# Kernel optimization log

Measured on AMD Instinct MI355X. Metric: run time of the kernel, lower is better.

The kernel has to match this reference:

```python
import jax, jax.numpy as jnp
import numpy as np

C = 16          # n_channels
HIDDEN = 128
ALPHA_THRESH = 0.1
STEP_SIZE = 1.0


def _perception_kernel():
    ident = jnp.array([[0., 0., 0.], [0., 1., 0.], [0., 0., 0.]], dtype=jnp.float32)
    dx = jnp.array([[-0.125, 0., 0.125], [-0.25, 0., 0.25], [-0.125, 0., 0.125]], dtype=jnp.float32)
    dy = dx.T  # angle = 0 -> no rotation
    k = jnp.stack([ident, dx, dy])                 # [3,3,3]
    return jnp.tile(k, (C, 1, 1))[:, None]          # [3C,1,3,3], OIHW, groups=C


def _wrap_pad(x):
    # circular padding of 1 on H and W (torus)
    return jnp.pad(x, ((0, 0), (0, 0), (1, 1), (1, 1)), mode='wrap')


def _living_mask(x):
    alpha = x[:, 3:4]                               # [B,1,H,W]
    pooled = jax.lax.reduce_window(_wrap_pad(alpha), -jnp.inf, jax.lax.max,
                                   (1, 1, 3, 3), (1, 1, 1, 1), 'VALID')
    return pooled > ALPHA_THRESH                    # [B,1,H,W] bool


def _perceive(x):
    kern = _perception_kernel()
    return jax.lax.conv_general_dilated(
        _wrap_pad(x), kern, window_strides=(1, 1), padding='VALID',
        feature_group_count=C,
        dimension_numbers=('NCHW', 'OIHW', 'NCHW'))   # [B,3C,H,W]


def setup_inputs() -> dict:
    key = jax.random.key(0)
    k1, k2, k3, k4 = jax.random.split(key, 4)
    B, H, W = 32, 256, 256
    x = jax.random.uniform(k1, (B, C, H, W), dtype=jnp.float32)
    fire_mask = jax.random.randint(k2, (B, 1, H, W), 0, 2).astype(jnp.int32)
    # Conv2d(48->128,1) and Conv2d(128->16,1) weights, stored as matrices
    w1 = jax.random.normal(k3, (HIDDEN, 3 * C), dtype=jnp.float32) * (1.0 / np.sqrt(3 * C))
    b1 = jnp.zeros((HIDDEN,), dtype=jnp.float32)
    w2 = jax.random.normal(k4, (C, HIDDEN), dtype=jnp.float32) * (1.0 / np.sqrt(HIDDEN))
    b2 = jnp.zeros((C,), dtype=jnp.float32)
    return {"x": x, "w1": w1, "b1": b1, "w2": w2, "b2": b2, "fire_mask": fire_mask}


def reference(x, w1, b1, w2, b2, fire_mask):
    pre_life = _living_mask(x)                                   # [B,1,H,W]
    y = _perceive(x)                                             # [B,3C,H,W]
    h = jax.nn.relu(jnp.einsum('bchw,oc->bohw', y, w1) + b1[None, :, None, None])
    dx = (jnp.einsum('bchw,oc->bohw', h, w2) + b2[None, :, None, None]) * STEP_SIZE
    dx = dx * fire_mask.astype(dx.dtype)                          # stochastic update mask
    x_new = x + dx
    post_life = _living_mask(x_new)
    life = (pre_life & post_life).astype(x_new.dtype)
    return x_new * life
```

## Files before the change

### kernel.cpp

```cpp
#include <hip/hip_runtime.h>
#include <hip/hip_bf16.h>


#define CCH 16
#define HID 128
#define HH 256
#define WW 256
#define BB 32

typedef __attribute__((ext_vector_type(8))) short bf16x8;
typedef __attribute__((ext_vector_type(4))) float f32x4;
typedef __attribute__((ext_vector_type(4))) int i32x4;
typedef __attribute__((ext_vector_type(2))) unsigned int u32x2;

union bfpack {
  u32x2 w2[2];
  bf16x8 v;
};

__device__ inline unsigned short f2bf(float f) {
  unsigned int u = __float_as_uint(f);
  u += 0x7FFFu + ((u >> 16) & 1u);
  return (unsigned short)(u >> 16);
}
__device__ inline float bf2f(unsigned short s) {
  return __uint_as_float(((unsigned int)s) << 16);
}
__device__ inline unsigned int cvtpk2(float a, float b) {
  union { __hip_bfloat162 h; unsigned int u; } cv;
  cv.h = __float22bfloat162_rn(make_float2(a, b));
  return cv.u;
}

__global__ __launch_bounds__(256) void pack_weights_kernel(
    const float* __restrict__ w1, const float* __restrict__ w2,
    unsigned short* __restrict__ w1p, unsigned short* __restrict__ w2p) {
  const int tid = blockIdx.x * 256 + threadIdx.x;
  if (tid < 2048) {
    const int l = tid & 63, m = (tid >> 6) & 7, ks = (tid >> 9) & 1,
              pl = (tid >> 10) & 1;
    const int row = m * 16 + (l & 15);
    const int kb = ks * 32 + (l >> 4) * 8;
    const size_t off = ((((size_t)pl * 2 + ks) * 8 + m) * 64 + l) * 8;
#pragma unroll
    for (int j = 0; j < 8; ++j) {
      const int k = kb + j;
      const int cc = k >> 2, f = k & 3;
      const float v = (f < 3) ? w1[row * 48 + cc * 3 + f] : 0.0f;
      const unsigned short hi = f2bf(v);
      w1p[off + j] = (pl == 0) ? hi : f2bf(v - bf2f(hi));
    }
  } else if (tid < 2560) {
    const int t2 = tid - 2048;
    const int l = t2 & 63, ks = (t2 >> 6) & 3, pl = (t2 >> 8) & 1;
    const int row = l & 15;
    const int kb = ks * 32 + (l >> 4) * 8;
    const size_t off = (((size_t)pl * 4 + ks) * 64 + l) * 8;
#pragma unroll
    for (int j = 0; j < 8; ++j) {
      const float v = w2[row * 128 + kb + j];
      const unsigned short hi = f2bf(v);
      w2p[off + j] = (pl == 0) ? hi : f2bf(v - bf2f(hi));
    }
  }
}

__device__ inline int swkey(int row) {
  return (((row >> 2) ^ ((row & 3) << 2)) & 15) << 3;
}

__global__ __launch_bounds__(256, 4) void nca_mfma_kernel(
    const float* __restrict__ x, const float* __restrict__ b1,
    const float* __restrict__ b2, const unsigned short* __restrict__ w1p,
    const unsigned short* __restrict__ w2p, const int* __restrict__ fire,
    float* __restrict__ out, float* __restrict__ alpha_ws,
    unsigned char* __restrict__ pre_ws) {
  __shared__ __align__(16) unsigned char smem[24576];
  unsigned char* Ys = smem;
  unsigned char* Hsm = smem + 8192;

  const int L = blockIdx.x;
  const int orig = ((L & 7) << 12) | (L >> 3);
  const int b = orig >> 10;
  const int h = (orig >> 2) & 255;
  const int wt = orig & 3;
  const int tid = threadIdx.x;
  const int wv = tid >> 6, lane = tid & 63, g = lane >> 4, ln = lane & 15;
  const int c = wv * 4 + g;
  const int q = ln;
  const int gcol0 = wt * 64 + q * 4;
  const int hm = (h + 255) & 255, hp = (h + 1) & 255;

  const float* xc = x + (size_t)(b * CCH + c) * (HH * WW);
  const f32x4 t4 = *(const f32x4*)(xc + (size_t)hm * WW + gcol0);
  const f32x4 m4 = *(const f32x4*)(xc + (size_t)h * WW + gcol0);
  const f32x4 o4 = *(const f32x4*)(xc + (size_t)hp * WW + gcol0);
  f32x4 av, bv;
#pragma unroll
  for (int j = 0; j < 4; ++j) {
    av[j] = 0.125f * (t4[j] + o4[j]) + 0.25f * m4[j];
    bv[j] = 0.125f * (o4[j] - t4[j]);
  }

  float haA = 0.f, haB = 0.f, hcm = 0.f;
  if (q == 0 || q == 15) {
    const int gc = (q == 15) ? ((wt * 64 + 64) & 255) : ((wt * 64 + 255) & 255);
    const float t = xc[(size_t)hm * WW + gc];
    const float m = xc[(size_t)h * WW + gc];
    const float bo = xc[(size_t)hp * WW + gc];
    haA = 0.125f * (t + bo) + 0.25f * m;
    haB = 0.125f * (bo - t);
    hcm = fmaxf(fmaxf(t, m), bo);
  }

  {
    float aLs = __shfl(av[3], lane - 1, 64);
    float bLs = __shfl(bv[3], lane - 1, 64);
    float aRs = __shfl(av[0], lane + 1, 64);
    float bRs = __shfl(bv[0], lane + 1, 64);
    if (q == 0) { aLs = haA; bLs = haB; }
    if (q == 15) { aRs = haA; bRs = haB; }

    const int c8 = c * 8;
#pragma unroll
    for (int i = 0; i < 4; ++i) {
      const float aR = (i < 3) ? av[i + 1] : aRs;
      const float aL = (i > 0) ? av[i - 1] : aLs;
      const float bR = (i < 3) ? bv[i + 1] : bRs;
      const float bL = (i > 0) ? bv[i - 1] : bLs;
      const float y0 = m4[i];
      const float y1 = aR - aL;
      const float y2 = bL + 2.0f * bv[i] + bR;
      const int px = q * 4 + i;
      u32x2 w;
      w[0] = cvtpk2(y0, y1);
      w[1] = cvtpk2(y2, 0.0f);
      *(u32x2*)(Ys + px * 128 + (c8 ^ swkey(px))) = w;
    }

    if (c == 3) {
      f32x4 cm4;
#pragma unroll
      for (int j = 0; j < 4; ++j) cm4[j] = fmaxf(fmaxf(t4[j], m4[j]), o4[j]);
      float cmL = __shfl(cm4[3], lane - 1, 64);
      float cmR = __shfl(cm4[0], lane + 1, 64);
      if (q == 0) cmL = hcm;
      if (q == 15) cmR = hcm;
      const float p0 = fmaxf(fmaxf(cmL, cm4[0]), cm4[1]);
      const float p1 = fmaxf(fmaxf(cm4[0], cm4[1]), cm4[2]);
      const float p2 = fmaxf(fmaxf(cm4[1], cm4[2]), cm4[3]);
      const float p3 = fmaxf(fmaxf(cm4[2], cm4[3]), cmR);
      const unsigned int pb = (p0 > 0.1f ? 1u : 0u) |
                              ((p1 > 0.1f ? 1u : 0u) << 8) |
                              ((p2 > 0.1f ? 1u : 0u) << 16) |
                              ((p3 > 0.1f ? 1u : 0u) << 24);
      const size_t pix0 = ((size_t)b * HH + h) * WW + gcol0;
      *(unsigned int*)(pre_ws + pix0) = pb;
    }
  }

  bf16x8 A1[2][4];
#pragma unroll
  for (int mi = 0; mi < 2; ++mi)
#pragma unroll
    for (int f = 0; f < 4; ++f)
      A1[mi][f] = *(const bf16x8*)(
          w1p + (((size_t)f * 8 + (wv * 2 + mi)) * 64 + lane) * 8);
  f32x4 b1v[2];
#pragma unroll
  for (int mi = 0; mi < 2; ++mi)
    b1v[mi] = *(const f32x4*)(b1 + (wv * 2 + mi) * 16 + g * 4);

  __syncthreads();

#pragma unroll
  for (int ni = 0; ni < 4; ++ni) {
    const int pxb = ni * 16 + ln;
    const int sk = swkey(pxb);
    const unsigned char* rb = Ys + pxb * 128;
    bfpack B0, B1;
    B0.w2[0] = *(const u32x2*)(rb + ((g * 16) ^ sk));
    B0.w2[1] = *(const u32x2*)(rb + ((g * 16 + 8) ^ sk));
    B1.w2[0] = *(const u32x2*)(rb + ((64 + g * 16) ^ sk));
    B1.w2[1] = *(const u32x2*)(rb + ((64 + g * 16 + 8) ^ sk));
#pragma unroll
    for (int mi = 0; mi < 2; ++mi) {
      f32x4 a = (f32x4){0.f, 0.f, 0.f, 0.f};
      a = __builtin_amdgcn_mfma_f32_16x16x32_bf16(A1[mi][0], B0.v, a, 0, 0, 0);
      a = __builtin_amdgcn_mfma_f32_16x16x32_bf16(A1[mi][1], B1.v, a, 0, 0, 0);
      a = __builtin_amdgcn_mfma_f32_16x16x32_bf16(A1[mi][2], B0.v, a, 0, 0, 0);
      a = __builtin_amdgcn_mfma_f32_16x16x32_bf16(A1[mi][3], B1.v, a, 0, 0, 0);
      const int hid0 = (wv * 2 + mi) * 16 + g * 4;
      u32x2 hv;
      hv[0] = cvtpk2(fmaxf(a[0] + b1v[mi][0], 0.f),
                     fmaxf(a[1] + b1v[mi][1], 0.f));
      hv[1] = cvtpk2(fmaxf(a[2] + b1v[mi][2], 0.f),
                     fmaxf(a[3] + b1v[mi][3], 0.f));
      *(u32x2*)(Hsm + pxb * 256 + ((hid0 * 2) ^ sk)) = hv;
    }
  }
  __syncthreads();

  {
    bf16x8 A2[8];
#pragma unroll
    for (int i = 0; i < 8; ++i)
      A2[i] = *(const bf16x8*)(w2p + ((size_t)i * 64 + lane) * 8);

    const int px0 = wv * 16 + g * 4;
    const int wg0 = wt * 64 + px0;
    const size_t pix0 = ((size_t)b * HH + h) * WW + wg0;
    const i32x4 fi = *(const i32x4*)(fire + pix0);
    const float b2v = b2[ln];
    const size_t xi0 = (((size_t)(b * CCH + ln)) * HH + h) * WW + wg0;
    const f32x4 xo = *(const f32x4*)(x + xi0);

    const int prow = wv * 16 + ln;
    const int sk = swkey(prow);
    const unsigned char* rb = Hsm + prow * 256;
    f32x4 a = (f32x4){0.f, 0.f, 0.f, 0.f};
#pragma unroll
    for (int ks = 0; ks < 4; ++ks) {
      const int o = ks * 64 + g * 16;
      bfpack Hf;
      Hf.w2[0] = *(const u32x2*)(rb + (o ^ sk));
      Hf.w2[1] = *(const u32x2*)(rb + ((o + 8) ^ sk));
      a = __builtin_amdgcn_mfma_f32_16x16x32_bf16(Hf.v, A2[ks], a, 0, 0, 0);
      a = __builtin_amdgcn_mfma_f32_16x16x32_bf16(Hf.v, A2[4 + ks], a, 0, 0, 0);
    }
    f32x4 v;
#pragma unroll
    for (int r = 0; r < 4; ++r) v[r] = xo[r] + (a[r] + b2v) * (float)fi[r];
    *(f32x4*)(out + xi0) = v;
    if (ln == 3) *(f32x4*)(alpha_ws + pix0) = v;
  }
}

__global__ __launch_bounds__(256) void life_mask_kernel(
    const float* __restrict__ alpha_ws, const unsigned char* __restrict__ pre_ws,
    float* __restrict__ out) {
  const int idx = blockIdx.x * 256 + threadIdx.x;
  const int lane = idx & 63;
  const int w0 = lane * 4;
  const int h = (idx >> 6) & 255;
  const int b = idx >> 14;
  const int hm = (h + 255) & 255;
  const int hp = (h + 1) & 255;

  const float* ab = alpha_ws + (size_t)b * HH * WW;
  const f32x4 up = *(const f32x4*)(ab + (size_t)hm * WW + w0);
  const f32x4 mi = *(const f32x4*)(ab + (size_t)h * WW + w0);
  const f32x4 dn = *(const f32x4*)(ab + (size_t)hp * WW + w0);
  f32x4 cm;
#pragma unroll
  for (int j = 0; j < 4; ++j) cm[j] = fmaxf(fmaxf(up[j], mi[j]), dn[j]);

  const float cmL = __shfl(cm[3], (lane + 63) & 63, 64);
  const float cmR = __shfl(cm[0], (lane + 1) & 63, 64);
  const float p0 = fmaxf(fmaxf(cmL, cm[0]), cm[1]);
  const float p1 = fmaxf(fmaxf(cm[0], cm[1]), cm[2]);
  const float p2 = fmaxf(fmaxf(cm[1], cm[2]), cm[3]);
  const float p3 = fmaxf(fmaxf(cm[2], cm[3]), cmR);

  const size_t pix0 = ((size_t)b * HH + h) * WW + w0;
  const unsigned int pb = *(const unsigned int*)(pre_ws + pix0);
  const bool l0 = (p0 > 0.1f) && (pb & 0xFFu);
  const bool l1 = (p1 > 0.1f) && (pb & 0xFF00u);
  const bool l2 = (p2 > 0.1f) && (pb & 0xFF0000u);
  const bool l3 = (p3 > 0.1f) && (pb & 0xFF000000u);

  if (!(l0 && l1 && l2 && l3)) {
    const bool lv[4] = {l0, l1, l2, l3};
#pragma unroll
    for (int r = 0; r < 4; ++r) {
      if (!lv[r]) {
        float* op = out + ((size_t)b * CCH * HH + h) * WW + w0 + r;
#pragma unroll
        for (int c = 0; c < CCH; ++c) op[(size_t)c * HH * WW] = 0.0f;
      }
    }
  }
}

extern "C" void kernel_launch(void* const* d_in, const int* in_sizes, int n_in,
                              void* d_out, int out_size, void* d_ws,
                              size_t ws_size, hipStream_t stream) {
  const float* x = (const float*)d_in[0];
  const float* w1 = (const float*)d_in[1];
  const float* b1 = (const float*)d_in[2];
  const float* w2 = (const float*)d_in[3];
  const float* b2 = (const float*)d_in[4];
  const int* fire = (const int*)d_in[5];
  float* out = (float*)d_out;

  const size_t npix = (size_t)BB * HH * WW;
  unsigned short* w1p = (unsigned short*)d_ws;
  unsigned short* w2p = (unsigned short*)((char*)d_ws + 32768);
  float* alpha_ws = (float*)((char*)d_ws + 40960);
  unsigned char* pre_ws = (unsigned char*)d_ws + 40960 + npix * sizeof(float);

  pack_weights_kernel<<<10, 256, 0, stream>>>(w1, w2, w1p, w2p);
  nca_mfma_kernel<<<BB * HH * 4, 256, 0, stream>>>(x, b1, b2, w1p, w2p, fire,
                                                   out, alpha_ws, pre_ws);
  life_mask_kernel<<<(int)(npix / 4 / 256), 256, 0, stream>>>(alpha_ws, pre_ws,
                                                              out);
}
```

Baseline: 172.7 us.

## Make NCA kernel persistent with prefetch of next tile's input rows

Replaces the one-block-per-tile launch with a persistent grid of 1536 blocks. Each block loops over tiles with stride 192 inside its XCD group. The three x rows for the next tile are loaded after the first barrier, while the current tile's MFMA work runs, so global latency can overlap compute. Launch bounds rise to 6 waves per SIMD to allow more resident blocks. This adds register pressure and a tail imbalance, and the weight fragments are still reloaded every iteration.

```diff
diff --git a/kernel.cpp b/kernel.cpp
--- a/kernel.cpp
+++ b/kernel.cpp
@@ -69,7 +69,7 @@
   return (((row >> 2) ^ ((row & 3) << 2)) & 15) << 3;
 }
 
-__global__ __launch_bounds__(256, 4) void nca_mfma_kernel(
+__global__ __launch_bounds__(256, 6) void nca_mfma_kernel(
     const float* __restrict__ x, const float* __restrict__ b1,
     const float* __restrict__ b2, const unsigned short* __restrict__ w1p,
     const unsigned short* __restrict__ w2p, const int* __restrict__ fire,
@@ -79,160 +79,189 @@
   unsigned char* Ys = smem;
   unsigned char* Hsm = smem + 8192;
 
-  const int L = blockIdx.x;
-  const int orig = ((L & 7) << 12) | (L >> 3);
-  const int b = orig >> 10;
-  const int h = (orig >> 2) & 255;
-  const int wt = orig & 3;
+  const int p = blockIdx.x;
+  const int xcd = p & 7;
+  const int slot = p >> 3;
   const int tid = threadIdx.x;
   const int wv = tid >> 6, lane = tid & 63, g = lane >> 4, ln = lane & 15;
   const int c = wv * 4 + g;
   const int q = ln;
-  const int gcol0 = wt * 64 + q * 4;
-  const int hm = (h + 255) & 255, hp = (h + 1) & 255;
-
-  const float* xc = x + (size_t)(b * CCH + c) * (HH * WW);
-  const f32x4 t4 = *(const f32x4*)(xc + (size_t)hm * WW + gcol0);
-  const f32x4 m4 = *(const f32x4*)(xc + (size_t)h * WW + gcol0);
-  const f32x4 o4 = *(const f32x4*)(xc + (size_t)hp * WW + gcol0);
-  f32x4 av, bv;
-#pragma unroll
-  for (int j = 0; j < 4; ++j) {
-    av[j] = 0.125f * (t4[j] + o4[j]) + 0.25f * m4[j];
-    bv[j] = 0.125f * (o4[j] - t4[j]);
+  const bool edge = (q == 0 || q == 15);
+
+  int b = ((xcd << 12) + slot) >> 10;
+  int h = (slot >> 2) & 255;
+  int wt = slot & 3;
+
+  f32x4 t4, m4, o4;
+  {
+    const float* xc = x + (size_t)(b * CCH + c) * (HH * WW);
+    const int gcol0 = wt * 64 + q * 4;
+    const int hmr = (h + 255) & 255, hpr = (h + 1) & 255;
+    t4 = *(const f32x4*)(xc + (size_t)hmr * WW + gcol0);
+    m4 = *(const f32x4*)(xc + (size_t)h * WW + gcol0);
+    o4 = *(const f32x4*)(xc + (size_t)hpr * WW + gcol0);
   }
 
-  float haA = 0.f, haB = 0.f, hcm = 0.f;
-  if (q == 0 || q == 15) {
-    const int gc = (q == 15) ? ((wt * 64 + 64) & 255) : ((wt * 64 + 255) & 255);
-    const float t = xc[(size_t)hm * WW + gc];
-    const float m = xc[(size_t)h * WW + gc];
-    const float bo = xc[(size_t)hp * WW + gc];
-    haA = 0.125f * (t + bo) + 0.25f * m;
-    haB = 0.125f * (bo - t);
-    hcm = fmaxf(fmaxf(t, m), bo);
-  }
-
-  {
-    float aLs = __shfl(av[3], lane - 1, 64);
-    float bLs = __shfl(bv[3], lane - 1, 64);
-    float aRs = __shfl(av[0], lane + 1, 64);
-    float bRs = __shfl(bv[0], lane + 1, 64);
-    if (q == 0) { aLs = haA; bLs = haB; }
-    if (q == 15) { aRs = haA; bRs = haB; }
-
-    const int c8 = c * 8;
-#pragma unroll
-    for (int i = 0; i < 4; ++i) {
-      const float aR = (i < 3) ? av[i + 1] : aRs;
-      const float aL = (i > 0) ? av[i - 1] : aLs;
-      const float bR = (i < 3) ? bv[i + 1] : bRs;
-      const float bL = (i > 0) ? bv[i - 1] : bLs;
-      const float y0 = m4[i];
-      const float y1 = aR - aL;
-      const float y2 = bL + 2.0f * bv[i] + bR;
-      const int px = q * 4 + i;
-      u32x2 w;
-      w[0] = cvtpk2(y0, y1);
-      w[1] = cvtpk2(y2, 0.0f);
-      *(u32x2*)(Ys + px * 128 + (c8 ^ swkey(px))) = w;
-    }
-
-    if (c == 3) {
-      f32x4 cm4;
-#pragma unroll
-      for (int j = 0; j < 4; ++j) cm4[j] = fmaxf(fmaxf(t4[j], m4[j]), o4[j]);
-      float cmL = __shfl(cm4[3], lane - 1, 64);
-      float cmR = __shfl(cm4[0], lane + 1, 64);
-      if (q == 0) cmL = hcm;
-      if (q == 15) cmR = hcm;
-      const float p0 = fmaxf(fmaxf(cmL, cm4[0]), cm4[1]);
-      const float p1 = fmaxf(fmaxf(cm4[0], cm4[1]), cm4[2]);
-      const float p2 = fmaxf(fmaxf(cm4[1], cm4[2]), cm4[3]);
-      const float p3 = fmaxf(fmaxf(cm4[2], cm4[3]), cmR);
-      const unsigned int pb = (p0 > 0.1f ? 1u : 0u) |
-                              ((p1 > 0.1f ? 1u : 0u) << 8) |
-                              ((p2 > 0.1f ? 1u : 0u) << 16) |
-                              ((p3 > 0.1f ? 1u : 0u) << 24);
-      const size_t pix0 = ((size_t)b * HH + h) * WW + gcol0;
-      *(unsigned int*)(pre_ws + pix0) = pb;
-    }
-  }
-
-  bf16x8 A1[2][4];
-#pragma unroll
-  for (int mi = 0; mi < 2; ++mi)
-#pragma unroll
-    for (int f = 0; f < 4; ++f)
-      A1[mi][f] = *(const bf16x8*)(
-          w1p + (((size_t)f * 8 + (wv * 2 + mi)) * 64 + lane) * 8);
-  f32x4 b1v[2];
-#pragma unroll
-  for (int mi = 0; mi < 2; ++mi)
-    b1v[mi] = *(const f32x4*)(b1 + (wv * 2 + mi) * 16 + g * 4);
-
-  __syncthreads();
-
-#pragma unroll
-  for (int ni = 0; ni < 4; ++ni) {
-    const int pxb = ni * 16 + ln;
-    const int sk = swkey(pxb);
-    const unsigned char* rb = Ys + pxb * 128;
-    bfpack B0, B1;
-    B0.w2[0] = *(const u32x2*)(rb + ((g * 16) ^ sk));
-    B0.w2[1] = *(const u32x2*)(rb + ((g * 16 + 8) ^ sk));
-    B1.w2[0] = *(const u32x2*)(rb + ((64 + g * 16) ^ sk));
-    B1.w2[1] = *(const u32x2*)(rb + ((64 + g * 16 + 8) ^ sk));
-#pragma unroll
-    for (int mi = 0; mi < 2; ++mi) {
+  for (int t = slot; t < 4096; t += 192) {
+    const int gcol0 = wt * 64 + q * 4;
+    const int hm = (h + 255) & 255, hp = (h + 1) & 255;
+    const float* xc = x + (size_t)(b * CCH + c) * (HH * WW);
+
+    f32x4 av, bv;
+#pragma unroll
+    for (int j = 0; j < 4; ++j) {
+      av[j] = 0.125f * (t4[j] + o4[j]) + 0.25f * m4[j];
+      bv[j] = 0.125f * (o4[j] - t4[j]);
+    }
+    float haA = 0.f, haB = 0.f, hcm = 0.f;
+    if (edge) {
+      const int gc =
+          (q == 15) ? ((wt * 64 + 64) & 255) : ((wt * 64 + 255) & 255);
+      const float tt = xc[(size_t)hm * WW + gc];
+      const float mm = xc[(size_t)h * WW + gc];
+      const float bo = xc[(size_t)hp * WW + gc];
+      haA = 0.125f * (tt + bo) + 0.25f * mm;
+      haB = 0.125f * (bo - tt);
+      hcm = fmaxf(fmaxf(tt, mm), bo);
+    }
+    {
+      float aLs = __shfl(av[3], lane - 1, 64);
+      float bLs = __shfl(bv[3], lane - 1, 64);
+      float aRs = __shfl(av[0], lane + 1, 64);
+      float bRs = __shfl(bv[0], lane + 1, 64);
+      if (q == 0) { aLs = haA; bLs = haB; }
+      if (q == 15) { aRs = haA; bRs = haB; }
+
+      const int c8 = c * 8;
+#pragma unroll
+      for (int i = 0; i < 4; ++i) {
+        const float aR = (i < 3) ? av[i + 1] : aRs;
+        const float aL = (i > 0) ? av[i - 1] : aLs;
+        const float bR = (i < 3) ? bv[i + 1] : bRs;
+        const float bL = (i > 0) ? bv[i - 1] : bLs;
+        const float y0 = m4[i];
+        const float y1 = aR - aL;
+        const float y2 = bL + 2.0f * bv[i] + bR;
+        const int px = q * 4 + i;
+        u32x2 w;
+        w[0] = cvtpk2(y0, y1);
+        w[1] = cvtpk2(y2, 0.0f);
+        *(u32x2*)(Ys + px * 128 + (c8 ^ swkey(px))) = w;
+      }
+
+      if (c == 3) {
+        f32x4 cm4;
+#pragma unroll
+        for (int j = 0; j < 4; ++j) cm4[j] = fmaxf(fmaxf(t4[j], m4[j]), o4[j]);
+        float cmL = __shfl(cm4[3], lane - 1, 64);
+        float cmR = __shfl(cm4[0], lane + 1, 64);
+        if (q == 0) cmL = hcm;
+        if (q == 15) cmR = hcm;
+        const float p0 = fmaxf(fmaxf(cmL, cm4[0]), cm4[1]);
+        const float p1 = fmaxf(fmaxf(cm4[0], cm4[1]), cm4[2]);
+        const float p2 = fmaxf(fmaxf(cm4[1], cm4[2]), cm4[3]);
+        const float p3 = fmaxf(fmaxf(cm4[2], cm4[3]), cmR);
+        const unsigned int pb = (p0 > 0.1f ? 1u : 0u) |
+                                ((p1 > 0.1f ? 1u : 0u) << 8) |
+                                ((p2 > 0.1f ? 1u : 0u) << 16) |
+                                ((p3 > 0.1f ? 1u : 0u) << 24);
+        const size_t pix0 = ((size_t)b * HH + h) * WW + gcol0;
+        *(unsigned int*)(pre_ws + pix0) = pb;
+      }
+    }
+
+    bf16x8 A1[2][4];
+#pragma unroll
+    for (int mi = 0; mi < 2; ++mi)
+#pragma unroll
+      for (int f = 0; f < 4; ++f)
+        A1[mi][f] = *(const bf16x8*)(
+            w1p + (((size_t)f * 8 + (wv * 2 + mi)) * 64 + lane) * 8);
+    f32x4 b1v[2];
+#pragma unroll
+    for (int mi = 0; mi < 2; ++mi)
+      b1v[mi] = *(const f32x4*)(b1 + (wv * 2 + mi) * 16 + g * 4);
+
+    __syncthreads();
+
+    const int tn = t + 192;
+    const int tv = (tn < 4096) ? tn : slot;
+    const int bn = ((xcd << 12) + tv) >> 10;
+    const int hn = (tv >> 2) & 255;
+    const int wtn = tv & 3;
+    {
+      const float* xc2 = x + (size_t)(bn * CCH + c) * (HH * WW);
+      const int gcol2 = wtn * 64 + q * 4;
+      const int hmr = (hn + 255) & 255, hpr = (hn + 1) & 255;
+      t4 = *(const f32x4*)(xc2 + (size_t)hmr * WW + gcol2);
+      m4 = *(const f32x4*)(xc2 + (size_t)hn * WW + gcol2);
+      o4 = *(const f32x4*)(xc2 + (size_t)hpr * WW + gcol2);
+    }
+    __builtin_amdgcn_sched_barrier(0);
+
+#pragma unroll
+    for (int ni = 0; ni < 4; ++ni) {
+      const int pxb = ni * 16 + ln;
+      const int sk = swkey(pxb);
+      const unsigned char* rb = Ys + pxb * 128;
+      bfpack B0, B1;
+      B0.w2[0] = *(const u32x2*)(rb + ((g * 16) ^ sk));
+      B0.w2[1] = *(const u32x2*)(rb + ((g * 16 + 8) ^ sk));
+      B1.w2[0] = *(const u32x2*)(rb + ((64 + g * 16) ^ sk));
+      B1.w2[1] = *(const u32x2*)(rb + ((64 + g * 16 + 8) ^ sk));
+#pragma unroll
+      for (int mi = 0; mi < 2; ++mi) {
+        f32x4 a = (f32x4){0.f, 0.f, 0.f, 0.f};
+        a = __builtin_amdgcn_mfma_f32_16x16x32_bf16(A1[mi][0], B0.v, a, 0, 0, 0);
+        a = __builtin_amdgcn_mfma_f32_16x16x32_bf16(A1[mi][1], B1.v, a, 0, 0, 0);
+        a = __builtin_amdgcn_mfma_f32_16x16x32_bf16(A1[mi][2], B0.v, a, 0, 0, 0);
+        a = __builtin_amdgcn_mfma_f32_16x16x32_bf16(A1[mi][3], B1.v, a, 0, 0, 0);
+        const int hid0 = (wv * 2 + mi) * 16 + g * 4;
+        u32x2 hv;
+        hv[0] = cvtpk2(fmaxf(a[0] + b1v[mi][0], 0.f),
+                       fmaxf(a[1] + b1v[mi][1], 0.f));
+        hv[1] = cvtpk2(fmaxf(a[2] + b1v[mi][2], 0.f),
+                       fmaxf(a[3] + b1v[mi][3], 0.f));
+        *(u32x2*)(Hsm + pxb * 256 + ((hid0 * 2) ^ sk)) = hv;
+      }
+    }
+    __syncthreads();
+
+    {
+      bf16x8 A2[8];
+#pragma unroll
+      for (int i = 0; i < 8; ++i)
+        A2[i] = *(const bf16x8*)(w2p + ((size_t)i * 64 + lane) * 8);
+
+      const int px0 = wv * 16 + g * 4;
+      const int wg0 = wt * 64 + px0;
+      const size_t pix0 = ((size_t)b * HH + h) * WW + wg0;
+      const i32x4 fi = *(const i32x4*)(fire + pix0);
+      const float b2v = b2[ln];
+      const size_t xi0 = (((size_t)(b * CCH + ln)) * HH + h) * WW + wg0;
+      const f32x4 xo = *(const f32x4*)(x + xi0);
+
+      const int prow = wv * 16 + ln;
+      const int sk = swkey(prow);
+      const unsigned char* rb = Hsm + prow * 256;
       f32x4 a = (f32x4){0.f, 0.f, 0.f, 0.f};
-      a = __builtin_amdgcn_mfma_f32_16x16x32_bf16(A1[mi][0], B0.v, a, 0, 0, 0);
-      a = __builtin_amdgcn_mfma_f32_16x16x32_bf16(A1[mi][1], B1.v, a, 0, 0, 0);
-      a = __builtin_amdgcn_mfma_f32_16x16x32_bf16(A1[mi][2], B0.v, a, 0, 0, 0);
-      a = __builtin_amdgcn_mfma_f32_16x16x32_bf16(A1[mi][3], B1.v, a, 0, 0, 0);
-      const int hid0 = (wv * 2 + mi) * 16 + g * 4;
-      u32x2 hv;
-      hv[0] = cvtpk2(fmaxf(a[0] + b1v[mi][0], 0.f),
-                     fmaxf(a[1] + b1v[mi][1], 0.f));
-      hv[1] = cvtpk2(fmaxf(a[2] + b1v[mi][2], 0.f),
-                     fmaxf(a[3] + b1v[mi][3], 0.f));
-      *(u32x2*)(Hsm + pxb * 256 + ((hid0 * 2) ^ sk)) = hv;
-    }
-  }
-  __syncthreads();
-
-  {
-    bf16x8 A2[8];
-#pragma unroll
-    for (int i = 0; i < 8; ++i)
-      A2[i] = *(const bf16x8*)(w2p + ((size_t)i * 64 + lane) * 8);
-
-    const int px0 = wv * 16 + g * 4;
-    const int wg0 = wt * 64 + px0;
-    const size_t pix0 = ((size_t)b * HH + h) * WW + wg0;
-    const i32x4 fi = *(const i32x4*)(fire + pix0);
-    const float b2v = b2[ln];
-    const size_t xi0 = (((size_t)(b * CCH + ln)) * HH + h) * WW + wg0;
-    const f32x4 xo = *(const f32x4*)(x + xi0);
-
-    const int prow = wv * 16 + ln;
-    const int sk = swkey(prow);
-    const unsigned char* rb = Hsm + prow * 256;
-    f32x4 a = (f32x4){0.f, 0.f, 0.f, 0.f};
-#pragma unroll
-    for (int ks = 0; ks < 4; ++ks) {
-      const int o = ks * 64 + g * 16;
-      bfpack Hf;
-      Hf.w2[0] = *(const u32x2*)(rb + (o ^ sk));
-      Hf.w2[1] = *(const u32x2*)(rb + ((o + 8) ^ sk));
-      a = __builtin_amdgcn_mfma_f32_16x16x32_bf16(Hf.v, A2[ks], a, 0, 0, 0);
-      a = __builtin_amdgcn_mfma_f32_16x16x32_bf16(Hf.v, A2[4 + ks], a, 0, 0, 0);
-    }
-    f32x4 v;
-#pragma unroll
-    for (int r = 0; r < 4; ++r) v[r] = xo[r] + (a[r] + b2v) * (float)fi[r];
-    *(f32x4*)(out + xi0) = v;
-    if (ln == 3) *(f32x4*)(alpha_ws + pix0) = v;
+#pragma unroll
+      for (int ks = 0; ks < 4; ++ks) {
+        const int o = ks * 64 + g * 16;
+        bfpack Hf;
+        Hf.w2[0] = *(const u32x2*)(rb + (o ^ sk));
+        Hf.w2[1] = *(const u32x2*)(rb + ((o + 8) ^ sk));
+        a = __builtin_amdgcn_mfma_f32_16x16x32_bf16(Hf.v, A2[ks], a, 0, 0, 0);
+        a = __builtin_amdgcn_mfma_f32_16x16x32_bf16(Hf.v, A2[4 + ks], a, 0, 0, 0);
+      }
+      f32x4 v;
+#pragma unroll
+      for (int r = 0; r < 4; ++r) v[r] = xo[r] + (a[r] + b2v) * (float)fi[r];
+      *(f32x4*)(out + xi0) = v;
+      if (ln == 3) *(f32x4*)(alpha_ws + pix0) = v;
+    }
+
+    b = bn; h = hn; wt = wtn;
   }
 }
 
@@ -300,8 +329,8 @@
   unsigned char* pre_ws = (unsigned char*)d_ws + 40960 + npix * sizeof(float);
 
   pack_weights_kernel<<<10, 256, 0, stream>>>(w1, w2, w1p, w2p);
-  nca_mfma_kernel<<<BB * HH * 4, 256, 0, stream>>>(x, b1, b2, w1p, w2p, fire,
-                                                   out, alpha_ws, pre_ws);
+  nca_mfma_kernel<<<1536, 256, 0, stream>>>(x, b1, b2, w1p, w2p, fire, out,
+                                            alpha_ws, pre_ws);
   life_mask_kernel<<<(int)(npix / 4 / 256), 256, 0, stream>>>(alpha_ws, pre_ws,
                                                               out);
 }
```

After: 463.4 us. 2.68x slower.

## Repartition first GEMM so each wave owns its pixels, dropping a block barrier

Applied to the files above, without the earlier changes.

Each wave now computes all 128 hidden channels for its own 16 pixels instead of 32 hidden channels for all 64 pixels. The wave therefore writes exactly the hidden rows its second GEMM reads, which removes the __syncthreads between the two GEMMs. The cost is that every wave loads all of W1 (8x4 fragments) and b1 per iteration rather than a quarter of them, which adds global/L2 traffic and register pressure. The MFMA count per wave is unchanged.

```diff
diff --git a/kernel.cpp b/kernel.cpp
--- a/kernel.cpp
+++ b/kernel.cpp
@@ -158,25 +158,11 @@
       *(unsigned int*)(pre_ws + pix0) = pb;
     }
   }
-
-  bf16x8 A1[2][4];
-#pragma unroll
-  for (int mi = 0; mi < 2; ++mi)
-#pragma unroll
-    for (int f = 0; f < 4; ++f)
-      A1[mi][f] = *(const bf16x8*)(
-          w1p + (((size_t)f * 8 + (wv * 2 + mi)) * 64 + lane) * 8);
-  f32x4 b1v[2];
-#pragma unroll
-  for (int mi = 0; mi < 2; ++mi)
-    b1v[mi] = *(const f32x4*)(b1 + (wv * 2 + mi) * 16 + g * 4);
-
   __syncthreads();
 
-#pragma unroll
-  for (int ni = 0; ni < 4; ++ni) {
-    const int pxb = ni * 16 + ln;
-    const int sk = swkey(pxb);
+  const int pxb = wv * 16 + ln;
+  const int sk = swkey(pxb);
+  {
     const unsigned char* rb = Ys + pxb * 128;
     bfpack B0, B1;
     B0.w2[0] = *(const u32x2*)(rb + ((g * 16) ^ sk));
@@ -184,22 +170,25 @@
     B1.w2[0] = *(const u32x2*)(rb + ((64 + g * 16) ^ sk));
     B1.w2[1] = *(const u32x2*)(rb + ((64 + g * 16 + 8) ^ sk));
 #pragma unroll
-    for (int mi = 0; mi < 2; ++mi) {
+    for (int mt = 0; mt < 8; ++mt) {
+      bf16x8 A1[4];
+#pragma unroll
+      for (int f = 0; f < 4; ++f)
+        A1[f] =
+            *(const bf16x8*)(w1p + (((size_t)f * 8 + mt) * 64 + lane) * 8);
+      const int hid0 = mt * 16 + g * 4;
+      const f32x4 b1v = *(const f32x4*)(b1 + hid0);
       f32x4 a = (f32x4){0.f, 0.f, 0.f, 0.f};
-      a = __builtin_amdgcn_mfma_f32_16x16x32_bf16(A1[mi][0], B0.v, a, 0, 0, 0);
-      a = __builtin_amdgcn_mfma_f32_16x16x32_bf16(A1[mi][1], B1.v, a, 0, 0, 0);
-      a = __builtin_amdgcn_mfma_f32_16x16x32_bf16(A1[mi][2], B0.v, a, 0, 0, 0);
-      a = __builtin_amdgcn_mfma_f32_16x16x32_bf16(A1[mi][3], B1.v, a, 0, 0, 0);
-      const int hid0 = (wv * 2 + mi) * 16 + g * 4;
+      a = __builtin_amdgcn_mfma_f32_16x16x32_bf16(A1[0], B0.v, a, 0, 0, 0);
+      a = __builtin_amdgcn_mfma_f32_16x16x32_bf16(A1[1], B1.v, a, 0, 0, 0);
+      a = __builtin_amdgcn_mfma_f32_16x16x32_bf16(A1[2], B0.v, a, 0, 0, 0);
+      a = __builtin_amdgcn_mfma_f32_16x16x32_bf16(A1[3], B1.v, a, 0, 0, 0);
       u32x2 hv;
-      hv[0] = cvtpk2(fmaxf(a[0] + b1v[mi][0], 0.f),
-                     fmaxf(a[1] + b1v[mi][1], 0.f));
-      hv[1] = cvtpk2(fmaxf(a[2] + b1v[mi][2], 0.f),
-                     fmaxf(a[3] + b1v[mi][3], 0.f));
+      hv[0] = cvtpk2(fmaxf(a[0] + b1v[0], 0.f), fmaxf(a[1] + b1v[1], 0.f));
+      hv[1] = cvtpk2(fmaxf(a[2] + b1v[2], 0.f), fmaxf(a[3] + b1v[3], 0.f));
       *(u32x2*)(Hsm + pxb * 256 + ((hid0 * 2) ^ sk)) = hv;
     }
   }
-  __syncthreads();
 
   {
     bf16x8 A2[8];
@@ -215,9 +204,7 @@
     const size_t xi0 = (((size_t)(b * CCH + ln)) * HH + h) * WW + wg0;
     const f32x4 xo = *(const f32x4*)(x + xi0);
 
-    const int prow = wv * 16 + ln;
-    const int sk = swkey(prow);
-    const unsigned char* rb = Hsm + prow * 256;
+    const unsigned char* rb = Hsm + pxb * 256;
     f32x4 a = (f32x4){0.f, 0.f, 0.f, 0.f};
 #pragma unroll
     for (int ks = 0; ks < 4; ++ks) {
```

New measurement: 257.7 us. 1.49x slower.

## Process two 64-pixel tiles per block and prefetch the second tile's perception

Applied to the files above, without the earlier changes.

Each block now handles two adjacent 64-column tiles instead of one, halving the grid size. The second tile's perception features are computed up front into registers, then written to shared memory after the first tile's first GEMM, so its global loads overlap that tile's work. The first layer's weight fragments and biases are loaded once and reused for both tiles. In exchange, register pressure rises and each block does more sequential work, which can reduce occupancy and parallel slack.

```diff
diff --git a/kernel.cpp b/kernel.cpp
--- a/kernel.cpp
+++ b/kernel.cpp
@@ -80,40 +80,42 @@
   unsigned char* Hsm = smem + 8192;
 
   const int L = blockIdx.x;
-  const int orig = ((L & 7) << 12) | (L >> 3);
-  const int b = orig >> 10;
-  const int h = (orig >> 2) & 255;
-  const int wt = orig & 3;
+  const int orig = ((L & 7) << 11) | (L >> 3);
+  const int b = orig >> 9;
+  const int h = (orig >> 1) & 255;
+  const int u = orig & 1;
+  const int wt1 = u * 2, wt2 = u * 2 + 1;
   const int tid = threadIdx.x;
   const int wv = tid >> 6, lane = tid & 63, g = lane >> 4, ln = lane & 15;
   const int c = wv * 4 + g;
   const int q = ln;
-  const int gcol0 = wt * 64 + q * 4;
   const int hm = (h + 255) & 255, hp = (h + 1) & 255;
-
   const float* xc = x + (size_t)(b * CCH + c) * (HH * WW);
-  const f32x4 t4 = *(const f32x4*)(xc + (size_t)hm * WW + gcol0);
-  const f32x4 m4 = *(const f32x4*)(xc + (size_t)h * WW + gcol0);
-  const f32x4 o4 = *(const f32x4*)(xc + (size_t)hp * WW + gcol0);
-  f32x4 av, bv;
-#pragma unroll
-  for (int j = 0; j < 4; ++j) {
-    av[j] = 0.125f * (t4[j] + o4[j]) + 0.25f * m4[j];
-    bv[j] = 0.125f * (o4[j] - t4[j]);
-  }
-
-  float haA = 0.f, haB = 0.f, hcm = 0.f;
-  if (q == 0 || q == 15) {
-    const int gc = (q == 15) ? ((wt * 64 + 64) & 255) : ((wt * 64 + 255) & 255);
-    const float t = xc[(size_t)hm * WW + gc];
-    const float m = xc[(size_t)h * WW + gc];
-    const float bo = xc[(size_t)hp * WW + gc];
-    haA = 0.125f * (t + bo) + 0.25f * m;
-    haB = 0.125f * (bo - t);
-    hcm = fmaxf(fmaxf(t, m), bo);
-  }
+
+  u32x2 yP[4];
 
   {
+    const int gcol0 = wt1 * 64 + q * 4;
+    const f32x4 t4 = *(const f32x4*)(xc + (size_t)hm * WW + gcol0);
+    const f32x4 m4 = *(const f32x4*)(xc + (size_t)h * WW + gcol0);
+    const f32x4 o4 = *(const f32x4*)(xc + (size_t)hp * WW + gcol0);
+    f32x4 av, bv;
+#pragma unroll
+    for (int j = 0; j < 4; ++j) {
+      av[j] = 0.125f * (t4[j] + o4[j]) + 0.25f * m4[j];
+      bv[j] = 0.125f * (o4[j] - t4[j]);
+    }
+    float haA = 0.f, haB = 0.f, hcm = 0.f;
+    if (q == 0 || q == 15) {
+      const int gc =
+          (q == 15) ? ((wt1 * 64 + 64) & 255) : ((wt1 * 64 + 255) & 255);
+      const float t = xc[(size_t)hm * WW + gc];
+      const float m = xc[(size_t)h * WW + gc];
+      const float bo = xc[(size_t)hp * WW + gc];
+      haA = 0.125f * (t + bo) + 0.25f * m;
+      haB = 0.125f * (bo - t);
+      hcm = fmaxf(fmaxf(t, m), bo);
+    }
     float aLs = __shfl(av[3], lane - 1, 64);
     float bLs = __shfl(bv[3], lane - 1, 64);
     float aRs = __shfl(av[0], lane + 1, 64);
@@ -128,16 +130,12 @@
       const float aL = (i > 0) ? av[i - 1] : aLs;
       const float bR = (i < 3) ? bv[i + 1] : bRs;
       const float bL = (i > 0) ? bv[i - 1] : bLs;
-      const float y0 = m4[i];
-      const float y1 = aR - aL;
-      const float y2 = bL + 2.0f * bv[i] + bR;
       const int px = q * 4 + i;
       u32x2 w;
-      w[0] = cvtpk2(y0, y1);
-      w[1] = cvtpk2(y2, 0.0f);
+      w[0] = cvtpk2(m4[i], aR - aL);
+      w[1] = cvtpk2(bL + 2.0f * bv[i] + bR, 0.0f);
       *(u32x2*)(Ys + px * 128 + (c8 ^ swkey(px))) = w;
     }
-
     if (c == 3) {
       f32x4 cm4;
 #pragma unroll
@@ -154,8 +152,65 @@
                               ((p1 > 0.1f ? 1u : 0u) << 8) |
                               ((p2 > 0.1f ? 1u : 0u) << 16) |
                               ((p3 > 0.1f ? 1u : 0u) << 24);
-      const size_t pix0 = ((size_t)b * HH + h) * WW + gcol0;
-      *(unsigned int*)(pre_ws + pix0) = pb;
+      *(unsigned int*)(pre_ws + ((size_t)b * HH + h) * WW + gcol0) = pb;
+    }
+  }
+
+  {
+    const int gcol0 = wt2 * 64 + q * 4;
+    const f32x4 t4 = *(const f32x4*)(xc + (size_t)hm * WW + gcol0);
+    const f32x4 m4 = *(const f32x4*)(xc + (size_t)h * WW + gcol0);
+    const f32x4 o4 = *(const f32x4*)(xc + (size_t)hp * WW + gcol0);
+    f32x4 av, bv;
+#pragma unroll
+    for (int j = 0; j < 4; ++j) {
+      av[j] = 0.125f * (t4[j] + o4[j]) + 0.25f * m4[j];
+      bv[j] = 0.125f * (o4[j] - t4[j]);
+    }
+    float haA = 0.f, haB = 0.f, hcm = 0.f;
+    if (q == 0 || q == 15) {
+      const int gc =
+          (q == 15) ? ((wt2 * 64 + 64) & 255) : ((wt2 * 64 + 255) & 255);
+      const float t = xc[(size_t)hm * WW + gc];
+      const float m = xc[(size_t)h * WW + gc];
+      const float bo = xc[(size_t)hp * WW + gc];
+      haA = 0.125f * (t + bo) + 0.25f * m;
+      haB = 0.125f * (bo - t);
+      hcm = fmaxf(fmaxf(t, m), bo);
+    }
+    float aLs = __shfl(av[3], lane - 1, 64);
+    float bLs = __shfl(bv[3], lane - 1, 64);
+    float aRs = __shfl(av[0], lane + 1, 64);
+    float bRs = __shfl(bv[0], lane + 1, 64);
+    if (q == 0) { aLs = haA; bLs = haB; }
+    if (q == 15) { aRs = haA; bRs = haB; }
+
+#pragma unroll
+    for (int i = 0; i < 4; ++i) {
+      const float aR = (i < 3) ? av[i + 1] : aRs;
+      const float aL = (i > 0) ? av[i - 1] : aLs;
+      const float bR = (i < 3) ? bv[i + 1] : bRs;
+      const float bL = (i > 0) ? bv[i - 1] : bLs;
+      yP[i][0] = cvtpk2(m4[i], aR - aL);
+      yP[i][1] = cvtpk2(bL + 2.0f * bv[i] + bR, 0.0f);
+    }
+    if (c == 3) {
+      f32x4 cm4;
+#pragma unroll
+      for (int j = 0; j < 4; ++j) cm4[j] = fmaxf(fmaxf(t4[j], m4[j]), o4[j]);
+      float cmL = __shfl(cm4[3], lane - 1, 64);
+      float cmR = __shfl(cm4[0], lane + 1, 64);
+      if (q == 0) cmL = hcm;
+      if (q == 15) cmR = hcm;
+      const float p0 = fmaxf(fmaxf(cmL, cm4[0]), cm4[1]);
+      const float p1 = fmaxf(fmaxf(cm4[0], cm4[1]), cm4[2]);
+      const float p2 = fmaxf(fmaxf(cm4[1], cm4[2]), cm4[3]);
+      const float p3 = fmaxf(fmaxf(cm4[2], cm4[3]), cmR);
+      const unsigned int pb = (p0 > 0.1f ? 1u : 0u) |
+                              ((p1 > 0.1f ? 1u : 0u) << 8) |
+                              ((p2 > 0.1f ? 1u : 0u) << 16) |
+                              ((p3 > 0.1f ? 1u : 0u) << 24);
+      *(unsigned int*)(pre_ws + ((size_t)b * HH + h) * WW + gcol0) = pb;
     }
   }
 
@@ -171,44 +226,43 @@
   for (int mi = 0; mi < 2; ++mi)
     b1v[mi] = *(const f32x4*)(b1 + (wv * 2 + mi) * 16 + g * 4);
 
-  __syncthreads();
-
-#pragma unroll
-  for (int ni = 0; ni < 4; ++ni) {
-    const int pxb = ni * 16 + ln;
-    const int sk = swkey(pxb);
-    const unsigned char* rb = Ys + pxb * 128;
-    bfpack B0, B1;
-    B0.w2[0] = *(const u32x2*)(rb + ((g * 16) ^ sk));
-    B0.w2[1] = *(const u32x2*)(rb + ((g * 16 + 8) ^ sk));
-    B1.w2[0] = *(const u32x2*)(rb + ((64 + g * 16) ^ sk));
-    B1.w2[1] = *(const u32x2*)(rb + ((64 + g * 16 + 8) ^ sk));
-#pragma unroll
-    for (int mi = 0; mi < 2; ++mi) {
-      f32x4 a = (f32x4){0.f, 0.f, 0.f, 0.f};
-      a = __builtin_amdgcn_mfma_f32_16x16x32_bf16(A1[mi][0], B0.v, a, 0, 0, 0);
-      a = __builtin_amdgcn_mfma_f32_16x16x32_bf16(A1[mi][1], B1.v, a, 0, 0, 0);
-      a = __builtin_amdgcn_mfma_f32_16x16x32_bf16(A1[mi][2], B0.v, a, 0, 0, 0);
-      a = __builtin_amdgcn_mfma_f32_16x16x32_bf16(A1[mi][3], B1.v, a, 0, 0, 0);
-      const int hid0 = (wv * 2 + mi) * 16 + g * 4;
-      u32x2 hv;
-      hv[0] = cvtpk2(fmaxf(a[0] + b1v[mi][0], 0.f),
-                     fmaxf(a[1] + b1v[mi][1], 0.f));
-      hv[1] = cvtpk2(fmaxf(a[2] + b1v[mi][2], 0.f),
-                     fmaxf(a[3] + b1v[mi][3], 0.f));
-      *(u32x2*)(Hsm + pxb * 256 + ((hid0 * 2) ^ sk)) = hv;
-    }
-  }
-  __syncthreads();
-
-  {
+  auto GEMM1 = [&]() {
+#pragma unroll
+    for (int ni = 0; ni < 4; ++ni) {
+      const int pxb = ni * 16 + ln;
+      const int sk = swkey(pxb);
+      const unsigned char* rb = Ys + pxb * 128;
+      bfpack B0, B1;
+      B0.w2[0] = *(const u32x2*)(rb + ((g * 16) ^ sk));
+      B0.w2[1] = *(const u32x2*)(rb + ((g * 16 + 8) ^ sk));
+      B1.w2[0] = *(const u32x2*)(rb + ((64 + g * 16) ^ sk));
+      B1.w2[1] = *(const u32x2*)(rb + ((64 + g * 16 + 8) ^ sk));
+#pragma unroll
+      for (int mi = 0; mi < 2; ++mi) {
+        f32x4 a = (f32x4){0.f, 0.f, 0.f, 0.f};
+        a = __builtin_amdgcn_mfma_f32_16x16x32_bf16(A1[mi][0], B0.v, a, 0, 0, 0);
+        a = __builtin_amdgcn_mfma_f32_16x16x32_bf16(A1[mi][1], B1.v, a, 0, 0, 0);
+        a = __builtin_amdgcn_mfma_f32_16x16x32_bf16(A1[mi][2], B0.v, a, 0, 0, 0);
+        a = __builtin_amdgcn_mfma_f32_16x16x32_bf16(A1[mi][3], B1.v, a, 0, 0, 0);
+        const int hid0 = (wv * 2 + mi) * 16 + g * 4;
+        u32x2 hv;
+        hv[0] = cvtpk2(fmaxf(a[0] + b1v[mi][0], 0.f),
+                       fmaxf(a[1] + b1v[mi][1], 0.f));
+        hv[1] = cvtpk2(fmaxf(a[2] + b1v[mi][2], 0.f),
+                       fmaxf(a[3] + b1v[mi][3], 0.f));
+        *(u32x2*)(Hsm + pxb * 256 + ((hid0 * 2) ^ sk)) = hv;
+      }
+    }
+  };
+
+  auto GEMM2 = [&](int wt_) {
     bf16x8 A2[8];
 #pragma unroll
     for (int i = 0; i < 8; ++i)
       A2[i] = *(const bf16x8*)(w2p + ((size_t)i * 64 + lane) * 8);
 
     const int px0 = wv * 16 + g * 4;
-    const int wg0 = wt * 64 + px0;
+    const int wg0 = wt_ * 64 + px0;
     const size_t pix0 = ((size_t)b * HH + h) * WW + wg0;
     const i32x4 fi = *(const i32x4*)(fire + pix0);
     const float b2v = b2[ln];
@@ -233,7 +287,24 @@
     for (int r = 0; r < 4; ++r) v[r] = xo[r] + (a[r] + b2v) * (float)fi[r];
     *(f32x4*)(out + xi0) = v;
     if (ln == 3) *(f32x4*)(alpha_ws + pix0) = v;
-  }
+  };
+
+  __syncthreads();
+  GEMM1();
+  __syncthreads();
+  {
+    const int c8 = c * 8;
+#pragma unroll
+    for (int i = 0; i < 4; ++i) {
+      const int px = q * 4 + i;
+      *(u32x2*)(Ys + px * 128 + (c8 ^ swkey(px))) = yP[i];
+    }
+  }
+  GEMM2(wt1);
+  __syncthreads();
+  GEMM1();
+  __syncthreads();
+  GEMM2(wt2);
 }
 
 __global__ __launch_bounds__(256) void life_mask_kernel(
@@ -300,7 +371,7 @@
   unsigned char* pre_ws = (unsigned char*)d_ws + 40960 + npix * sizeof(float);
 
   pack_weights_kernel<<<10, 256, 0, stream>>>(w1, w2, w1p, w2p);
-  nca_mfma_kernel<<<BB * HH * 4, 256, 0, stream>>>(x, b1, b2, w1p, w2p, fire,
+  nca_mfma_kernel<<<BB * HH * 2, 256, 0, stream>>>(x, b1, b2, w1p, w2p, fire,
                                                    out, alpha_ws, pre_ws);
   life_mask_kernel<<<(int)(npix / 4 / 256), 256, 0, stream>>>(alpha_ws, pre_ws,
                                                               out);
```

After: 172.6 us. About the same (-0.1%).
